# Kernel tuning notes

Hardware: AMD Instinct MI355X
Metric: run time of the kernel (lower is better)

Reference implementation:

```python
import jax, jax.numpy as jnp
import numpy as np

HEADS = 8
DIM_HEAD = 64
SCALE = DIM_HEAD ** -0.5


def setup_inputs() -> dict:
    key = jax.random.key(0)
    ks = jax.random.split(key, 8)
    B, Nq, Dq = 4, 2048, 512
    Nk, Dc = 1024, 768
    inner = HEADS * DIM_HEAD  # 512
    x = jax.random.normal(ks[0], (B, Nq, Dq), dtype=jnp.float32)
    context = jax.random.normal(ks[1], (B, Nk, Dc), dtype=jnp.float32)
    # Linear weights stored [in, out]; y = x @ W (+ b)
    Wq = jax.random.normal(ks[2], (Dq, inner), dtype=jnp.float32) / np.sqrt(Dq)
    Wk = jax.random.normal(ks[3], (Dc, inner), dtype=jnp.float32) / np.sqrt(Dc)
    Wv = jax.random.normal(ks[4], (Dc, inner), dtype=jnp.float32) / np.sqrt(Dc)
    Wo = jax.random.normal(ks[5], (inner, Dq), dtype=jnp.float32) / np.sqrt(inner)
    bo = jax.random.normal(ks[6], (Dq,), dtype=jnp.float32) * 0.01
    return {"x": x, "context": context, "Wq": Wq, "Wk": Wk, "Wv": Wv, "Wo": Wo, "bo": bo}


def reference(x, context, Wq, Wk, Wv, Wo, bo):
    B, Nq, _ = x.shape
    Nk = context.shape[1]
    # projections
    q = x @ Wq          # [B, Nq, h*d]
    k = context @ Wk    # [B, Nk, h*d]
    v = context @ Wv    # [B, Nk, h*d]
    # split heads: b n (h d) -> b h n d
    q = q.reshape(B, Nq, HEADS, DIM_HEAD).transpose(0, 2, 1, 3)
    k = k.reshape(B, Nk, HEADS, DIM_HEAD).transpose(0, 2, 1, 3)
    v = v.reshape(B, Nk, HEADS, DIM_HEAD).transpose(0, 2, 1, 3)
    # fp32 QK^T (ATTN_PRECISION == 'fp32' path)
    sim = jnp.einsum('bhid,bhjd->bhij', q.astype(jnp.float32), k.astype(jnp.float32)) * SCALE
    attn = jax.nn.softmax(sim, axis=-1)
    out = jnp.einsum('bhij,bhjd->bhid', attn, v)  # [B, h, Nq, d]
    out = out.transpose(0, 2, 1, 3).reshape(B, Nq, HEADS * DIM_HEAD)
    return out @ Wo + bo  # dropout=0 -> identity
```

## Files before the change

kernel.cpp:

```cpp
#include <hip/hip_runtime.h>
#include <cstddef>
#include <cstdint>

typedef __attribute__((ext_vector_type(8))) short bf16x8;
typedef __attribute__((ext_vector_type(4))) float f32x4;

static __device__ __forceinline__ short f2bf(float f) {
    union { float f; unsigned u; } x;
    x.f = f;
    unsigned r = (x.u + 0x7FFFu + ((x.u >> 16) & 1u)) >> 16;
    return (short)r;
}
static __device__ __forceinline__ short f2bf_fast(float f) {
    union { float f; unsigned u; } x;
    x.f = f;
    return (short)((x.u + 0x8000u) >> 16);
}

typedef __attribute__((address_space(3))) unsigned lds_u;
typedef const __attribute__((address_space(1))) unsigned glb_u;
static __device__ __forceinline__ void gld_lds16(const void* g, void* l) {
    __builtin_amdgcn_global_load_lds((glb_u*)g, (lds_u*)l, 16, 0, 0);
}

__global__ __launch_bounds__(256) void prep_kernel(
    const float* __restrict__ x, const float* __restrict__ c,
    const float* __restrict__ Wq, const float* __restrict__ Wk,
    const float* __restrict__ Wv, const float* __restrict__ Wo,
    short* __restrict__ xb, short* __restrict__ cb,
    short* __restrict__ wqT, short* __restrict__ wkvT, short* __restrict__ woT)
{
    const int bid = blockIdx.x;
    const int tid = threadIdx.x;
    if (bid < 7168) {
        int i = bid * 256 + tid;
        int nn1 = (8192 * 512) >> 2;
        const float* src; short* dst; int off;
        if (i < nn1) { src = x; dst = xb; off = i; }
        else { src = c; dst = cb; off = i - nn1; }
        float4 v = ((const float4*)src)[off];
        ushort4 w;
        w.x = (unsigned short)f2bf(v.x); w.y = (unsigned short)f2bf(v.y);
        w.z = (unsigned short)f2bf(v.z); w.w = (unsigned short)f2bf(v.w);
        ((ushort4*)dst)[off] = w;
        return;
    }
    __shared__ float T[32][33];
    int w = bid - 7168;
    const float* src; short* dst; int R, t;
    if (w < 256)       { src = Wq; dst = wqT;  R = 512; t = w; }
    else if (w < 640)  { src = Wk; dst = wkvT; R = 768; t = w - 256; }
    else if (w < 1024) { src = Wv; dst = wkvT + (size_t)512 * 768; R = 768; t = w - 640; }
    else               { src = Wo; dst = woT;  R = 512; t = w - 1024; }
    const int xt = t & 15, yt = t >> 4;
    {
        int r = tid >> 3, c4 = (tid & 7) * 4;
        float4 v = *(const float4*)&src[(size_t)(yt * 32 + r) * 512 + xt * 32 + c4];
        T[r][c4] = v.x; T[r][c4 + 1] = v.y; T[r][c4 + 2] = v.z; T[r][c4 + 3] = v.w;
    }
    __syncthreads();
    {
        int cc = tid >> 3, r4 = (tid & 7) * 4;
        ushort4 o;
        o.x = (unsigned short)f2bf(T[r4][cc]);     o.y = (unsigned short)f2bf(T[r4 + 1][cc]);
        o.z = (unsigned short)f2bf(T[r4 + 2][cc]); o.w = (unsigned short)f2bf(T[r4 + 3][cc]);
        *(ushort4*)&dst[(size_t)(xt * 32 + cc) * R + yt * 32 + r4] = o;
    }
}

__global__ __launch_bounds__(256) void vtrans_kernel(
    const short* __restrict__ v, short* __restrict__ vT)
{
    __shared__ short T[32][33];
    const int b = blockIdx.z, yt = blockIdx.y, xt = blockIdx.x;
    const int tid = threadIdx.x;
    {
        int r = tid >> 3, c4 = (tid & 7) * 4;
        ushort4 vv = *(const ushort4*)&v[((size_t)(b * 1024 + yt * 32 + r)) * 1024 + xt * 32 + c4];
        T[r][c4] = (short)vv.x; T[r][c4 + 1] = (short)vv.y;
        T[r][c4 + 2] = (short)vv.z; T[r][c4 + 3] = (short)vv.w;
    }
    __syncthreads();
    {
        int cc = tid >> 3, r4 = (tid & 7) * 4;
        ushort4 w;
        w.x = (unsigned short)T[r4][cc];     w.y = (unsigned short)T[r4 + 1][cc];
        w.z = (unsigned short)T[r4 + 2][cc]; w.w = (unsigned short)T[r4 + 3][cc];
        *(ushort4*)&vT[((size_t)(b * 512 + xt * 32 + cc)) * 1024 + yt * 32 + r4] = w;
    }
}

static __device__ __forceinline__ void gemm_hyb(
    const short* __restrict__ A, const short* __restrict__ BT, int K,
    int bm, int bn, short* As, f32x4 acc[4][4])
{
    const int tid = threadIdx.x, lane = tid & 63, wave = tid >> 6;
    const int lm = lane & 15, quad = lane >> 4;
    const int wm = (wave >> 1) * 64, wn = (wave & 1) * 64;
    const int cs = tid >> 7, rs = tid & 127;

    const short* Ag = A + (size_t)(bm + rs) * K;
    const short* Bb = BT + (size_t)(bn + wn + lm) * K + quad * 8;
    const size_t rsB = (size_t)16 * K;

    #pragma unroll
    for (int p = 0; p < 4; ++p)
        gld_lds16(Ag + (cs + 2 * p) * 8, As + ((cs + 2 * p) * 128 + rs) * 8);
    bf16x8 b0[4], b1[4], b2[4];
    #pragma unroll
    for (int j = 0; j < 4; ++j) b0[j] = *(const bf16x8*)(Bb + j * rsB);

    const int nw = K >> 6;
    for (int w = 0; w < nw; ++w) {
        short* Ac = As + (w & 1) * 8192;
        __syncthreads();
        if (w + 1 < nw) {
            short* An = As + ((w + 1) & 1) * 8192;
            const short* Agn = Ag + (w + 1) * 64;
            #pragma unroll
            for (int p = 0; p < 4; ++p)
                gld_lds16(Agn + (cs + 2 * p) * 8, An + ((cs + 2 * p) * 128 + rs) * 8);
        }
        #pragma unroll
        for (int j = 0; j < 4; ++j)
            b1[j] = *(const bf16x8*)(Bb + w * 64 + 32 + j * rsB);
        #pragma unroll
        for (int i = 0; i < 4; ++i) {
            bf16x8 af = *(const bf16x8*)&Ac[(quad * 128 + wm + i * 16 + lm) * 8];
            #pragma unroll
            for (int j = 0; j < 4; ++j)
                acc[i][j] = __builtin_amdgcn_mfma_f32_16x16x32_bf16(af, b0[j], acc[i][j], 0, 0, 0);
        }
        if (w + 1 < nw) {
            #pragma unroll
            for (int j = 0; j < 4; ++j)
                b2[j] = *(const bf16x8*)(Bb + (w + 1) * 64 + j * rsB);
        }
        #pragma unroll
        for (int i = 0; i < 4; ++i) {
            bf16x8 af = *(const bf16x8*)&Ac[((4 + quad) * 128 + wm + i * 16 + lm) * 8];
            #pragma unroll
            for (int j = 0; j < 4; ++j)
                acc[i][j] = __builtin_amdgcn_mfma_f32_16x16x32_bf16(af, b1[j], acc[i][j], 0, 0, 0);
        }
        #pragma unroll
        for (int j = 0; j < 4; ++j) b0[j] = b2[j];
    }
}

__global__ __launch_bounds__(256) void qkv_kernel(
    const short* __restrict__ xb, const short* __restrict__ cb,
    const short* __restrict__ wqT, const short* __restrict__ wkvT,
    short* __restrict__ qb, short* __restrict__ kvb)
{
    __shared__ short As[2 * 8192];
    const int bid = blockIdx.x;
    const short *A, *BT; short* C; int K, ldc, bm, bn;
    if (bid < 256) { A = xb; BT = wqT;  C = qb;  K = 512; ldc = 512;
                     bm = (bid >> 2) * 128; bn = (bid & 3) * 128; }
    else { int b2 = bid - 256; A = cb; BT = wkvT; C = kvb; K = 768; ldc = 1024;
           bm = (b2 >> 3) * 128; bn = (b2 & 7) * 128; }

    f32x4 acc[4][4] = {};
    gemm_hyb(A, BT, K, bm, bn, As, acc);

    const int lane = threadIdx.x & 63, wave = threadIdx.x >> 6;
    const int lm = lane & 15, quad = lane >> 4;
    const int wm = (wave >> 1) * 64, wn = (wave & 1) * 64;
    #pragma unroll
    for (int j = 0; j < 4; ++j) {
        int col = bn + wn + j * 16 + lm;
        #pragma unroll
        for (int i = 0; i < 4; ++i) {
            int row0 = bm + wm + i * 16 + quad * 4;
            #pragma unroll
            for (int r = 0; r < 4; ++r)
                C[(size_t)(row0 + r) * ldc + col] = f2bf(acc[i][j][r]);
        }
    }
}

__global__ __launch_bounds__(256) void ogemm_kernel(
    const short* __restrict__ ob, const short* __restrict__ woT,
    const float* __restrict__ bias, float* __restrict__ out)
{
    __shared__ short As[2 * 8192];
    const int bid = blockIdx.x;
    const int bm = (bid >> 2) * 128, bn = (bid & 3) * 128;

    f32x4 acc[4][4] = {};
    gemm_hyb(ob, woT, 512, bm, bn, As, acc);

    const int lane = threadIdx.x & 63, wave = threadIdx.x >> 6;
    const int lm = lane & 15, quad = lane >> 4;
    const int wm = (wave >> 1) * 64, wn = (wave & 1) * 64;
    #pragma unroll
    for (int j = 0; j < 4; ++j) {
        int col = bn + wn + j * 16 + lm;
        float bv = bias[col];
        #pragma unroll
        for (int i = 0; i < 4; ++i) {
            int row0 = bm + wm + i * 16 + quad * 4;
            #pragma unroll
            for (int r = 0; r < 4; ++r)
                out[(size_t)(row0 + r) * 512 + col] = acc[i][j][r] + bv;
        }
    }
}

__global__ __launch_bounds__(256) void attn_kernel(
    const short* __restrict__ q, const short* __restrict__ k,
    const short* __restrict__ vT, short* __restrict__ o)
{
    __shared__ short Qs[4096];
    __shared__ short Ks[2 * 4096];
    __shared__ short Vs[2 * 4096];

    const int tid  = threadIdx.x;
    const int lane = tid & 63;
    const int wave = tid >> 6;
    const int lm   = lane & 15;
    const int quad = lane >> 4;
    const int qt = blockIdx.x, h = blockIdx.y, b = blockIdx.z;
    const size_t qrow0 = (size_t)b * 2048 + qt * 64;
    const size_t krow0 = (size_t)b * 1024;
    const int hcol = h * 64;
    const size_t vrow0 = ((size_t)b * 8 + h) * 64;

    #pragma unroll
    for (int p = 0; p < 2; ++p) {
        int idx = p * 256 + tid;
        int c = idx >> 6, r = idx & 63;
        gld_lds16(&q[(qrow0 + r) * 512 + hcol + c * 8], &Qs[idx * 8]);
        gld_lds16(&k[(krow0 + r) * 1024 + hcol + c * 8], &Ks[idx * 8]);
        gld_lds16(&vT[(vrow0 + r) * 1024 + c * 8], &Vs[idx * 8]);
    }
    __syncthreads();
    bf16x8 qf0 = *(const bf16x8*)&Qs[((0 + quad) * 64 + wave * 16 + lm) * 8];
    bf16x8 qf1 = *(const bf16x8*)&Qs[((4 + quad) * 64 + wave * 16 + lm) * 8];

    short* Pw = &Qs[wave * 1024];
    const int pr0 = lm * 64 + ((quad ^ (lm & 7)) << 3);
    const int pr1 = lm * 64 + (((quad + 4) ^ (lm & 7)) << 3);

    constexpr float C1 = 0.18033688f;
    constexpr float C2 = 11.5415603f;

    f32x4 oacc[4] = {};
    float lrow[4] = {0.0f, 0.0f, 0.0f, 0.0f};

    for (int t = 0; t < 16; ++t) {
        const short* Kc = &Ks[(t & 1) * 4096];
        const short* Vc = &Vs[(t & 1) * 4096];
        __syncthreads();
        if (t + 1 < 16) {
            short* Kn = &Ks[((t + 1) & 1) * 4096];
            short* Vn = &Vs[((t + 1) & 1) * 4096];
            #pragma unroll
            for (int p = 0; p < 2; ++p) {
                int idx = p * 256 + tid;
                int c = idx >> 6, r = idx & 63;
                gld_lds16(&k[(krow0 + (t + 1) * 64 + r) * 1024 + hcol + c * 8], &Kn[idx * 8]);
                gld_lds16(&vT[(vrow0 + r) * 1024 + (t + 1) * 64 + c * 8], &Vn[idx * 8]);
            }
        }

        f32x4 sacc[4] = {};
        #pragma unroll
        for (int j = 0; j < 4; ++j) {
            bf16x8 kf0 = *(const bf16x8*)&Kc[((0 + quad) * 64 + j * 16 + lm) * 8];
            bf16x8 kf1 = *(const bf16x8*)&Kc[((4 + quad) * 64 + j * 16 + lm) * 8];
            sacc[j] = __builtin_amdgcn_mfma_f32_16x16x32_bf16(qf0, kf0, sacc[j], 0, 0, 0);
            sacc[j] = __builtin_amdgcn_mfma_f32_16x16x32_bf16(qf1, kf1, sacc[j], 0, 0, 0);
        }

        #pragma unroll
        for (int r = 0; r < 4; ++r) {
            int row = quad * 4 + r;
            int rsw = (row & 7);
            float lsum = 0.0f;
            #pragma unroll
            for (int j = 0; j < 4; ++j) {
                float pv = exp2f(fmaf(sacc[j][r], C1, -C2));
                lsum += pv;
                int cc = (2 * j + (lm >> 3)) ^ rsw;
                Pw[row * 64 + (cc << 3) + (lm & 7)] = f2bf_fast(pv);
            }
            lrow[r] += lsum;
        }
        bf16x8 pf0 = *(const bf16x8*)&Pw[pr0];
        bf16x8 pf1 = *(const bf16x8*)&Pw[pr1];

        #pragma unroll
        for (int j = 0; j < 4; ++j) {
            bf16x8 vf0 = *(const bf16x8*)&Vc[((0 + quad) * 64 + j * 16 + lm) * 8];
            bf16x8 vf1 = *(const bf16x8*)&Vc[((4 + quad) * 64 + j * 16 + lm) * 8];
            oacc[j] = __builtin_amdgcn_mfma_f32_16x16x32_bf16(pf0, vf0, oacc[j], 0, 0, 0);
            oacc[j] = __builtin_amdgcn_mfma_f32_16x16x32_bf16(pf1, vf1, oacc[j], 0, 0, 0);
        }
    }

    float inv[4];
    #pragma unroll
    for (int r = 0; r < 4; ++r) {
        float s = lrow[r];
        #pragma unroll
        for (int d = 1; d < 16; d <<= 1) s += __shfl_xor(s, d);
        inv[r] = 1.0f / s;
    }
    #pragma unroll
    for (int j = 0; j < 4; ++j) {
        int col = hcol + j * 16 + lm;
        #pragma unroll
        for (int r = 0; r < 4; ++r) {
            size_t row = qrow0 + wave * 16 + quad * 4 + r;
            o[row * 512 + col] = f2bf(oacc[j][r] * inv[r]);
        }
    }
}

extern "C" void kernel_launch(void* const* d_in, const int* in_sizes, int n_in,
                              void* d_out, int out_size, void* d_ws, size_t ws_size,
                              hipStream_t stream)
{
    const float* x   = (const float*)d_in[0];
    const float* ctx = (const float*)d_in[1];
    const float* Wq  = (const float*)d_in[2];
    const float* Wk  = (const float*)d_in[3];
    const float* Wv  = (const float*)d_in[4];
    const float* Wo  = (const float*)d_in[5];
    const float* bo  = (const float*)d_in[6];

    char* ws = (char*)d_ws;
    short* xb   = (short*)(ws);
    short* cb   = (short*)(ws + (8u << 20));
    short* wqT  = (short*)(ws + (14u << 20));
    short* wkvT = (short*)(ws + (14u << 20) + (512u << 10));
    short* woT  = (short*)(ws + (16u << 20));
    short* qb   = (short*)(ws + (16u << 20) + (512u << 10));
    short* kvb  = (short*)(ws + (24u << 20) + (512u << 10));
    short* ob   = xb;
    short* vT   = cb;

    prep_kernel<<<8448, 256, 0, stream>>>(x, ctx, Wq, Wk, Wv, Wo,
                                          xb, cb, wqT, wkvT, woT);
    qkv_kernel<<<512, 256, 0, stream>>>(xb, cb, wqT, wkvT, qb, kvb);
    vtrans_kernel<<<dim3(16, 32, 4), 256, 0, stream>>>(kvb + 512, vT);
    attn_kernel<<<dim3(32, 8, 4), 256, 0, stream>>>(qb, kvb, vT, ob);
    ogemm_kernel<<<256, 256, 0, stream>>>(ob, woT, bo, (float*)d_out);
}
```

Baseline: 192.4 us.

## Fuse Q projection into attention, V transpose into KV GEMM, shrink GEMM tiles

Computes the Q projection inside the attention kernel, loading x and Wq rows directly from global memory, and writes Q into the per-wave P buffer so the qb round trip disappears. The separate V transpose kernel is folded into the KV GEMM epilogue through an LDS transpose, which removes one launch and one pass over V. GEMM tiles shrink from 128x128 to 64x64 so more blocks launch. In exchange, every head block recomputes its Q slice from global loads without LDS reuse, and the smaller tiles get less operand reuse.

```diff
diff --git a/kernel.cpp b/kernel.cpp
--- a/kernel.cpp
+++ b/kernel.cpp
@@ -68,115 +68,94 @@
     }
 }
 
-__global__ __launch_bounds__(256) void vtrans_kernel(
-    const short* __restrict__ v, short* __restrict__ vT)
-{
-    __shared__ short T[32][33];
-    const int b = blockIdx.z, yt = blockIdx.y, xt = blockIdx.x;
-    const int tid = threadIdx.x;
-    {
-        int r = tid >> 3, c4 = (tid & 7) * 4;
-        ushort4 vv = *(const ushort4*)&v[((size_t)(b * 1024 + yt * 32 + r)) * 1024 + xt * 32 + c4];
-        T[r][c4] = (short)vv.x; T[r][c4 + 1] = (short)vv.y;
-        T[r][c4 + 2] = (short)vv.z; T[r][c4 + 3] = (short)vv.w;
-    }
-    __syncthreads();
-    {
-        int cc = tid >> 3, r4 = (tid & 7) * 4;
-        ushort4 w;
-        w.x = (unsigned short)T[r4][cc];     w.y = (unsigned short)T[r4 + 1][cc];
-        w.z = (unsigned short)T[r4 + 2][cc]; w.w = (unsigned short)T[r4 + 3][cc];
-        *(ushort4*)&vT[((size_t)(b * 512 + xt * 32 + cc)) * 1024 + yt * 32 + r4] = w;
-    }
-}
-
-static __device__ __forceinline__ void gemm_hyb(
+static __device__ __forceinline__ void gemm64_core(
     const short* __restrict__ A, const short* __restrict__ BT, int K,
-    int bm, int bn, short* As, f32x4 acc[4][4])
+    int bm, int bn, short* As, f32x4 acc[4])
 {
     const int tid = threadIdx.x, lane = tid & 63, wave = tid >> 6;
     const int lm = lane & 15, quad = lane >> 4;
-    const int wm = (wave >> 1) * 64, wn = (wave & 1) * 64;
-    const int cs = tid >> 7, rs = tid & 127;
+    const int cs = tid >> 6, rs = tid & 63;
 
     const short* Ag = A + (size_t)(bm + rs) * K;
-    const short* Bb = BT + (size_t)(bn + wn + lm) * K + quad * 8;
+    const short* Bb = BT + (size_t)(bn + lm) * K + quad * 8;
     const size_t rsB = (size_t)16 * K;
 
-    #pragma unroll
-    for (int p = 0; p < 4; ++p)
-        gld_lds16(Ag + (cs + 2 * p) * 8, As + ((cs + 2 * p) * 128 + rs) * 8);
+    gld_lds16(Ag + cs * 8,       As + (cs * 64 + rs) * 8);
+    gld_lds16(Ag + (cs + 4) * 8, As + ((cs + 4) * 64 + rs) * 8);
     bf16x8 b0[4], b1[4], b2[4];
     #pragma unroll
     for (int j = 0; j < 4; ++j) b0[j] = *(const bf16x8*)(Bb + j * rsB);
 
     const int nw = K >> 6;
     for (int w = 0; w < nw; ++w) {
-        short* Ac = As + (w & 1) * 8192;
+        short* Ac = As + (w & 1) * 4096;
         __syncthreads();
         if (w + 1 < nw) {
-            short* An = As + ((w + 1) & 1) * 8192;
+            short* An = As + ((w + 1) & 1) * 4096;
             const short* Agn = Ag + (w + 1) * 64;
-            #pragma unroll
-            for (int p = 0; p < 4; ++p)
-                gld_lds16(Agn + (cs + 2 * p) * 8, An + ((cs + 2 * p) * 128 + rs) * 8);
+            gld_lds16(Agn + cs * 8,       An + (cs * 64 + rs) * 8);
+            gld_lds16(Agn + (cs + 4) * 8, An + ((cs + 4) * 64 + rs) * 8);
         }
         #pragma unroll
         for (int j = 0; j < 4; ++j)
             b1[j] = *(const bf16x8*)(Bb + w * 64 + 32 + j * rsB);
-        #pragma unroll
-        for (int i = 0; i < 4; ++i) {
-            bf16x8 af = *(const bf16x8*)&Ac[(quad * 128 + wm + i * 16 + lm) * 8];
-            #pragma unroll
-            for (int j = 0; j < 4; ++j)
-                acc[i][j] = __builtin_amdgcn_mfma_f32_16x16x32_bf16(af, b0[j], acc[i][j], 0, 0, 0);
-        }
+        bf16x8 af0 = *(const bf16x8*)&Ac[(quad * 64 + wave * 16 + lm) * 8];
+        #pragma unroll
+        for (int j = 0; j < 4; ++j)
+            acc[j] = __builtin_amdgcn_mfma_f32_16x16x32_bf16(af0, b0[j], acc[j], 0, 0, 0);
         if (w + 1 < nw) {
             #pragma unroll
             for (int j = 0; j < 4; ++j)
                 b2[j] = *(const bf16x8*)(Bb + (w + 1) * 64 + j * rsB);
         }
-        #pragma unroll
-        for (int i = 0; i < 4; ++i) {
-            bf16x8 af = *(const bf16x8*)&Ac[((4 + quad) * 128 + wm + i * 16 + lm) * 8];
-            #pragma unroll
-            for (int j = 0; j < 4; ++j)
-                acc[i][j] = __builtin_amdgcn_mfma_f32_16x16x32_bf16(af, b1[j], acc[i][j], 0, 0, 0);
-        }
+        bf16x8 af1 = *(const bf16x8*)&Ac[((4 + quad) * 64 + wave * 16 + lm) * 8];
+        #pragma unroll
+        for (int j = 0; j < 4; ++j)
+            acc[j] = __builtin_amdgcn_mfma_f32_16x16x32_bf16(af1, b1[j], acc[j], 0, 0, 0);
         #pragma unroll
         for (int j = 0; j < 4; ++j) b0[j] = b2[j];
     }
 }
 
-__global__ __launch_bounds__(256) void qkv_kernel(
-    const short* __restrict__ xb, const short* __restrict__ cb,
-    const short* __restrict__ wqT, const short* __restrict__ wkvT,
-    short* __restrict__ qb, short* __restrict__ kvb)
-{
-    __shared__ short As[2 * 8192];
+__global__ __launch_bounds__(256) void kvgemm_kernel(
+    const short* __restrict__ cb, const short* __restrict__ wkvT,
+    short* __restrict__ kb, short* __restrict__ vT)
+{
+    __shared__ short As[2 * 4096];
     const int bid = blockIdx.x;
-    const short *A, *BT; short* C; int K, ldc, bm, bn;
-    if (bid < 256) { A = xb; BT = wqT;  C = qb;  K = 512; ldc = 512;
-                     bm = (bid >> 2) * 128; bn = (bid & 3) * 128; }
-    else { int b2 = bid - 256; A = cb; BT = wkvT; C = kvb; K = 768; ldc = 1024;
-           bm = (b2 >> 3) * 128; bn = (b2 & 7) * 128; }
-
-    f32x4 acc[4][4] = {};
-    gemm_hyb(A, BT, K, bm, bn, As, acc);
-
-    const int lane = threadIdx.x & 63, wave = threadIdx.x >> 6;
+    const int bm = (bid >> 4) * 64, bn = (bid & 15) * 64;
+
+    f32x4 acc[4] = {};
+    gemm64_core(cb, wkvT, 768, bm, bn, As, acc);
+
+    const int tid = threadIdx.x, lane = tid & 63, wave = tid >> 6;
     const int lm = lane & 15, quad = lane >> 4;
-    const int wm = (wave >> 1) * 64, wn = (wave & 1) * 64;
-    #pragma unroll
-    for (int j = 0; j < 4; ++j) {
-        int col = bn + wn + j * 16 + lm;
-        #pragma unroll
-        for (int i = 0; i < 4; ++i) {
-            int row0 = bm + wm + i * 16 + quad * 4;
+
+    if (bn < 512) {
+        #pragma unroll
+        for (int j = 0; j < 4; ++j) {
+            int col = bn + j * 16 + lm;
             #pragma unroll
             for (int r = 0; r < 4; ++r)
-                C[(size_t)(row0 + r) * ldc + col] = f2bf(acc[i][j][r]);
-        }
+                kb[(size_t)(bm + wave * 16 + quad * 4 + r) * 512 + col] = f2bf(acc[j][r]);
+        }
+    } else {
+        short* T = As;
+        __syncthreads();
+        #pragma unroll
+        for (int j = 0; j < 4; ++j)
+            #pragma unroll
+            for (int r = 0; r < 4; ++r)
+                T[(wave * 16 + quad * 4 + r) * 72 + j * 16 + lm] = f2bf(acc[j][r]);
+        __syncthreads();
+        const int d = tid >> 2, kv0 = (tid & 3) * 16;
+        short vals[16];
+        #pragma unroll
+        for (int i = 0; i < 16; ++i) vals[i] = T[(kv0 + i) * 72 + d];
+        const int b = bm >> 10;
+        size_t base = ((size_t)(b * 512 + (bn - 512) + d)) * 1024 + (bm & 1023) + kv0;
+        *(bf16x8*)&vT[base]     = *(bf16x8*)&vals[0];
+        *(bf16x8*)&vT[base + 8] = *(bf16x8*)&vals[8];
     }
 }
 
@@ -184,33 +163,29 @@
     const short* __restrict__ ob, const short* __restrict__ woT,
     const float* __restrict__ bias, float* __restrict__ out)
 {
-    __shared__ short As[2 * 8192];
+    __shared__ short As[2 * 4096];
     const int bid = blockIdx.x;
-    const int bm = (bid >> 2) * 128, bn = (bid & 3) * 128;
-
-    f32x4 acc[4][4] = {};
-    gemm_hyb(ob, woT, 512, bm, bn, As, acc);
+    const int bm = (bid >> 3) * 64, bn = (bid & 7) * 64;
+
+    f32x4 acc[4] = {};
+    gemm64_core(ob, woT, 512, bm, bn, As, acc);
 
     const int lane = threadIdx.x & 63, wave = threadIdx.x >> 6;
     const int lm = lane & 15, quad = lane >> 4;
-    const int wm = (wave >> 1) * 64, wn = (wave & 1) * 64;
     #pragma unroll
     for (int j = 0; j < 4; ++j) {
-        int col = bn + wn + j * 16 + lm;
+        int col = bn + j * 16 + lm;
         float bv = bias[col];
         #pragma unroll
-        for (int i = 0; i < 4; ++i) {
-            int row0 = bm + wm + i * 16 + quad * 4;
-            #pragma unroll
-            for (int r = 0; r < 4; ++r)
-                out[(size_t)(row0 + r) * 512 + col] = acc[i][j][r] + bv;
-        }
+        for (int r = 0; r < 4; ++r)
+            out[(size_t)(bm + wave * 16 + quad * 4 + r) * 512 + col] = acc[j][r] + bv;
     }
 }
 
 __global__ __launch_bounds__(256) void attn_kernel(
-    const short* __restrict__ q, const short* __restrict__ k,
-    const short* __restrict__ vT, short* __restrict__ o)
+    const short* __restrict__ xb, const short* __restrict__ wqT,
+    const short* __restrict__ kb, const short* __restrict__ vT,
+    short* __restrict__ o)
 {
     __shared__ short Qs[4096];
     __shared__ short Ks[2 * 4096];
@@ -231,17 +206,54 @@
     for (int p = 0; p < 2; ++p) {
         int idx = p * 256 + tid;
         int c = idx >> 6, r = idx & 63;
-        gld_lds16(&q[(qrow0 + r) * 512 + hcol + c * 8], &Qs[idx * 8]);
-        gld_lds16(&k[(krow0 + r) * 1024 + hcol + c * 8], &Ks[idx * 8]);
+        gld_lds16(&kb[(krow0 + r) * 512 + hcol + c * 8], &Ks[idx * 8]);
         gld_lds16(&vT[(vrow0 + r) * 1024 + c * 8], &Vs[idx * 8]);
     }
-    __syncthreads();
-    bf16x8 qf0 = *(const bf16x8*)&Qs[((0 + quad) * 64 + wave * 16 + lm) * 8];
-    bf16x8 qf1 = *(const bf16x8*)&Qs[((4 + quad) * 64 + wave * 16 + lm) * 8];
 
     short* Pw = &Qs[wave * 1024];
     const int pr0 = lm * 64 + ((quad ^ (lm & 7)) << 3);
     const int pr1 = lm * 64 + (((quad + 4) ^ (lm & 7)) << 3);
+    int rowo[4], swz[4];
+    #pragma unroll
+    for (int r = 0; r < 4; ++r) {
+        int row = quad * 4 + r;
+        rowo[r] = row * 64 + (lm & 7);
+        swz[r]  = row & 7;
+    }
+
+    {
+        const short* Axp = xb + (qrow0 + wave * 16 + lm) * 512 + quad * 8;
+        const short* Bqp = wqT + (size_t)(hcol + lm) * 512 + quad * 8;
+        f32x4 qacc[4] = {};
+        bf16x8 a0 = *(const bf16x8*)Axp;
+        bf16x8 bq[4], bqn[4];
+        #pragma unroll
+        for (int j = 0; j < 4; ++j) bq[j] = *(const bf16x8*)(Bqp + (size_t)j * 16 * 512);
+        bf16x8 a1;
+        for (int kk = 0; kk < 16; ++kk) {
+            if (kk + 1 < 16) {
+                a1 = *(const bf16x8*)(Axp + (kk + 1) * 32);
+                #pragma unroll
+                for (int j = 0; j < 4; ++j)
+                    bqn[j] = *(const bf16x8*)(Bqp + (kk + 1) * 32 + (size_t)j * 16 * 512);
+            }
+            #pragma unroll
+            for (int j = 0; j < 4; ++j)
+                qacc[j] = __builtin_amdgcn_mfma_f32_16x16x32_bf16(a0, bq[j], qacc[j], 0, 0, 0);
+            a0 = a1;
+            #pragma unroll
+            for (int j = 0; j < 4; ++j) bq[j] = bqn[j];
+        }
+        #pragma unroll
+        for (int r = 0; r < 4; ++r)
+            #pragma unroll
+            for (int j = 0; j < 4; ++j) {
+                int cc = (2 * j + (lm >> 3)) ^ swz[r];
+                Pw[rowo[r] + (cc << 3)] = f2bf(qacc[j][r]);
+            }
+    }
+    bf16x8 qf0 = *(const bf16x8*)&Pw[pr0];
+    bf16x8 qf1 = *(const bf16x8*)&Pw[pr1];
 
     constexpr float C1 = 0.18033688f;
     constexpr float C2 = 11.5415603f;
@@ -260,7 +272,7 @@
             for (int p = 0; p < 2; ++p) {
                 int idx = p * 256 + tid;
                 int c = idx >> 6, r = idx & 63;
-                gld_lds16(&k[(krow0 + (t + 1) * 64 + r) * 1024 + hcol + c * 8], &Kn[idx * 8]);
+                gld_lds16(&kb[(krow0 + (t + 1) * 64 + r) * 512 + hcol + c * 8], &Kn[idx * 8]);
                 gld_lds16(&vT[(vrow0 + r) * 1024 + (t + 1) * 64 + c * 8], &Vn[idx * 8]);
             }
         }
@@ -276,15 +288,13 @@
 
         #pragma unroll
         for (int r = 0; r < 4; ++r) {
-            int row = quad * 4 + r;
-            int rsw = (row & 7);
             float lsum = 0.0f;
             #pragma unroll
             for (int j = 0; j < 4; ++j) {
                 float pv = exp2f(fmaf(sacc[j][r], C1, -C2));
                 lsum += pv;
-                int cc = (2 * j + (lm >> 3)) ^ rsw;
-                Pw[row * 64 + (cc << 3) + (lm & 7)] = f2bf_fast(pv);
+                int cc = (2 * j + (lm >> 3)) ^ swz[r];
+                Pw[rowo[r] + (cc << 3)] = f2bf_fast(pv);
             }
             lrow[r] += lsum;
         }
@@ -337,15 +347,13 @@
     short* wqT  = (short*)(ws + (14u << 20));
     short* wkvT = (short*)(ws + (14u << 20) + (512u << 10));
     short* woT  = (short*)(ws + (16u << 20));
-    short* qb   = (short*)(ws + (16u << 20) + (512u << 10));
-    short* kvb  = (short*)(ws + (24u << 20) + (512u << 10));
-    short* ob   = xb;
-    short* vT   = cb;
+    short* kb   = (short*)(ws + (16u << 20) + (512u << 10));
+    short* vT   = (short*)(ws + (20u << 20) + (512u << 10));
+    short* ob   = (short*)(ws + (24u << 20) + (512u << 10));
 
     prep_kernel<<<8448, 256, 0, stream>>>(x, ctx, Wq, Wk, Wv, Wo,
                                           xb, cb, wqT, wkvT, woT);
-    qkv_kernel<<<512, 256, 0, stream>>>(xb, cb, wqT, wkvT, qb, kvb);
-    vtrans_kernel<<<dim3(16, 32, 4), 256, 0, stream>>>(kvb + 512, vT);
-    attn_kernel<<<dim3(32, 8, 4), 256, 0, stream>>>(qb, kvb, vT, ob);
-    ogemm_kernel<<<256, 256, 0, stream>>>(ob, woT, bo, (float*)d_out);
-}
+    kvgemm_kernel<<<1024, 256, 0, stream>>>(cb, wkvT, kb, vT);
+    attn_kernel<<<dim3(32, 8, 4), 256, 0, stream>>>(xb, wqT, kb, vT, ob);
+    ogemm_kernel<<<1024, 256, 0, stream>>>(ob, woT, bo, (float*)d_out);
+}
```

New measurement: 262.7 us. 1.37x slower.
